# Optimization experiments

Hardware: AMD Instinct MI355X
Metric: run time of the kernel (lower is better)

Reference implementation:

```python
import jax, jax.numpy as jnp
import numpy as np

N = 8388608          # number of samples (2**23)
T_MAX = 100000       # number of distinct time values -> ~84 ties per time


def setup_inputs() -> dict:
    key = jax.random.key(0)
    k1, k2, k3 = jax.random.split(key, 3)
    inp = jax.random.normal(k1, (N,), dtype=jnp.float32)            # log hazards
    target = jax.random.randint(k2, (N,), 0, T_MAX, dtype=jnp.int32)  # times
    weight = jax.random.randint(k3, (N,), 0, 2, dtype=jnp.int32)      # event indicator
    return {"input": inp, "target": target, "weight": weight}


def _cox_efron_npll(log_hz, time, event):
    """Negative Cox partial log-likelihood with Efron tie correction, mean reduction.

    Faithful to torchsurv's _partial_likelihood_efron: per unique time j,
    pll_j = sum_{i in H_j} log_hz_i - sum_{l=0}^{m_j-1} log(D_j - (l/m_j)*T_j)
    where H_j = events at time j, D_j = sum of exp(log_hz) over risk set (t>=t_j),
    T_j = sum of exp(log_hz) over H_j, m_j = |H_j|; loss = -mean over j with m_j>0.
    """
    n = log_hz.shape[0]
    order = jnp.argsort(time)                       # sort by time (group-sum math is tie-order invariant)
    t = time[order]
    lh = log_hz[order]
    ev = event[order].astype(lh.dtype)

    # group id per sample: 0..(num_unique-1), padded groups beyond that are empty
    new_grp = jnp.concatenate([jnp.zeros((1,), jnp.int32), (t[1:] != t[:-1]).astype(jnp.int32)])
    seg = jnp.cumsum(new_grp)                       # [n] int32

    hz = jnp.exp(lh)
    grp_hz = jax.ops.segment_sum(hz, seg, num_segments=n)          # sum exp per time group
    denom_naive = jnp.cumsum(grp_hz[::-1])[::-1]                   # risk-set sums (suffix over groups)
    m = jax.ops.segment_sum(ev, seg, num_segments=n)               # events per group
    log_nom = jax.ops.segment_sum(lh * ev, seg, num_segments=n)    # sum of log_hz over H_j
    ties = jax.ops.segment_sum(hz * ev, seg, num_segments=n)       # sum of exp over H_j

    # rank l in [0, m_j) of each event within its group
    csum_e = jnp.cumsum(ev)
    events_before = jnp.concatenate([jnp.zeros((1,), lh.dtype), jnp.cumsum(m)[:-1]])
    rank = csum_e - 1.0 - events_before[seg]
    mg = jnp.maximum(m[seg], 1.0)
    term = jnp.where(ev > 0.0,
                     jnp.log(denom_naive[seg] - (rank / mg) * ties[seg]),
                     0.0)
    log_denom = jax.ops.segment_sum(term, seg, num_segments=n)

    include = (m > 0.0).astype(lh.dtype)
    pll = jnp.where(m > 0.0, log_nom - log_denom, 0.0)
    # reduction='mean': -pll.nanmean() over groups that contain events
    return -(jnp.sum(pll) / jnp.sum(include))


def reference(input, target, weight):
    return _cox_efron_npll(input, target, weight)
```

## Files before the change

### kernel.cpp

```cpp
#include <hip/hip_runtime.h>

#define TMAXV 100000
#define CHUNK 256
#define NCHUNK ((TMAXV + CHUNK - 1) / CHUNK)
#define WB 512
#define LOGWB 9
#define SB ((TMAXV + WB - 1) / WB)
#define SBP 256
#define TILE 4096
#define RPT 16
#define KS 8
#define NREP 2
#define HSCALE 4096.0f
#define HINV (1.0f / 4096.0f)
#define CAPB 49152


__device__ __forceinline__ float block_reduce_sum(float v, float* sdata) {
    int lane = threadIdx.x & 63;
    int wid  = threadIdx.x >> 6;
    #pragma unroll
    for (int off = 32; off > 0; off >>= 1)
        v += __shfl_down(v, off, 64);
    if (lane == 0) sdata[wid] = v;
    __syncthreads();
    if (wid == 0) {
        v = (lane < 4) ? sdata[lane] : 0.0f;
        v += __shfl_down(v, 2, 64);
        v += __shfl_down(v, 1, 64);
    }
    return v;
}

__device__ __forceinline__ double block_reduce_sum_d(double v, double* sdata) {
    int lane = threadIdx.x & 63;
    int wid  = threadIdx.x >> 6;
    #pragma unroll
    for (int off = 32; off > 0; off >>= 1)
        v += __shfl_down(v, off, 64);
    if (lane == 0) sdata[wid] = v;
    __syncthreads();
    if (wid == 0) {
        v = (lane < 4) ? sdata[lane] : 0.0;
        v += __shfl_down(v, 2, 64);
        v += __shfl_down(v, 1, 64);
    }
    return v;
}

__device__ __forceinline__ unsigned encode_rec(float x, int t, int e) {
    float h = __expf(x);
    unsigned hf = (unsigned)__float2uint_rn(h * HSCALE);
    if (hf > 0x3FFFFFu) hf = 0x3FFFFFu;
    return (hf << 9)
         | (unsigned)(t & (WB - 1))
         | ((unsigned)e << 31);
}


__global__ void scatter_kernel(const float* __restrict__ lh,
                               const int*   __restrict__ tgt,
                               const int*   __restrict__ ev,
                               int*      __restrict__ gcnt,
                               unsigned* __restrict__ val,
                               double*   __restrict__ acc,
                               unsigned* __restrict__ zero_base,
                               int nzero_dw, int n) {
    __shared__ unsigned fu[TILE];
    __shared__ unsigned char bidv[TILE];
    __shared__ int cnl[SBP];
    __shared__ int tb[SBP];
    __shared__ int lrank[SBP];
    __shared__ int ls[SBP];
    __shared__ float sdata[4];
    int tid  = threadIdx.x;
    int tile = blockIdx.x;

    for (int i = tile * 256 + tid; i < nzero_dw; i += gridDim.x * 256)
        zero_base[i] = 0u;

    cnl[tid] = 0; lrank[tid] = 0;
    __syncthreads();

    int lo = tile * TILE;
    int cnt_here = min(TILE, n - lo);

    if (lo + TILE <= n) {
        const int4* tgt4 = (const int4*)(tgt + lo);
        #pragma unroll
        for (int q = 0; q < RPT / 4; ++q) {
            int4 t4 = tgt4[q * 256 + tid];
            atomicAdd(&cnl[t4.x >> LOGWB], 1);
            atomicAdd(&cnl[t4.y >> LOGWB], 1);
            atomicAdd(&cnl[t4.z >> LOGWB], 1);
            atomicAdd(&cnl[t4.w >> LOGWB], 1);
        }
    } else {
        for (int i = lo + tid; i < lo + cnt_here; i += 256)
            atomicAdd(&cnl[tgt[i] >> LOGWB], 1);
    }
    __syncthreads();

    int c0 = cnl[tid];
    ls[tid] = c0;
    __syncthreads();
    for (int off = 1; off < SBP; off <<= 1) {
        int a = (tid >= off) ? ls[tid - off] : 0;
        __syncthreads();
        ls[tid] += a;
        __syncthreads();
    }
    int pfxv = ls[tid] - c0;
    int res = 0;
    if (c0 > 0) {
        res = atomicAdd(&gcnt[tid * 16], c0);
        if (res > CAPB) res = CAPB;
    }
    cnl[tid] = pfxv;
    tb[tid]  = tid * CAPB + res - pfxv;
    __syncthreads();

    float xl = 0.f;
    if (lo + TILE <= n) {
        const int4*   tgt4 = (const int4*)(tgt + lo);
        const int4*   ev4  = (const int4*)(ev + lo);
        const float4* lh4  = (const float4*)(lh + lo);
        #pragma unroll
        for (int q = 0; q < RPT / 4; ++q) {
            int idx = q * 256 + tid;
            int4   t4 = tgt4[idx];
            int4   e4 = ev4[idx];
            float4 x4 = lh4[idx];
            {
                int b = t4.x >> LOGWB; unsigned r = encode_rec(x4.x, t4.x, e4.x & 1);
                int k = atomicAdd(&lrank[b], 1); int pos = cnl[b] + k;
                fu[pos] = r; bidv[pos] = (unsigned char)b; if (e4.x & 1) xl += x4.x;
            }
            {
                int b = t4.y >> LOGWB; unsigned r = encode_rec(x4.y, t4.y, e4.y & 1);
                int k = atomicAdd(&lrank[b], 1); int pos = cnl[b] + k;
                fu[pos] = r; bidv[pos] = (unsigned char)b; if (e4.y & 1) xl += x4.y;
            }
            {
                int b = t4.z >> LOGWB; unsigned r = encode_rec(x4.z, t4.z, e4.z & 1);
                int k = atomicAdd(&lrank[b], 1); int pos = cnl[b] + k;
                fu[pos] = r; bidv[pos] = (unsigned char)b; if (e4.z & 1) xl += x4.z;
            }
            {
                int b = t4.w >> LOGWB; unsigned r = encode_rec(x4.w, t4.w, e4.w & 1);
                int k = atomicAdd(&lrank[b], 1); int pos = cnl[b] + k;
                fu[pos] = r; bidv[pos] = (unsigned char)b; if (e4.w & 1) xl += x4.w;
            }
        }
    } else {
        for (int i = lo + tid; i < lo + cnt_here; i += 256) {
            int t = tgt[i]; int e = ev[i] & 1; float x = lh[i];
            int b = t >> LOGWB; unsigned r = encode_rec(x, t, e);
            int rr = atomicAdd(&lrank[b], 1); int pos = cnl[b] + rr;
            fu[pos] = r; bidv[pos] = (unsigned char)b; if (e) xl += x;
        }
    }
    __syncthreads();

    int pairs = cnt_here >> 1;
    const uint2* fu2 = (const uint2*)fu;
    for (int q = tid; q < pairs; q += 256) {
        uint2 bb = fu2[q];
        int p0 = q * 2;
        int b0 = (int)bidv[p0];
        int b1 = (int)bidv[p0 + 1];
        val[tb[b0] + p0]     = bb.x;
        val[tb[b1] + p0 + 1] = bb.y;
    }
    if ((cnt_here & 1) && tid == 0) {
        int p = cnt_here - 1;
        int b = (int)bidv[p];
        val[tb[b] + p] = fu[p];
    }

    float rl = block_reduce_sum(xl, sdata);
    if (tid == 0) unsafeAtomicAdd(&acc[2], (double)rl);
}

__global__ void bucket_hist_kernel(const unsigned* __restrict__ val,
                                   const int* __restrict__ gcnt,
                                   unsigned* __restrict__ sh_g,
                                   unsigned* __restrict__ cm_g,
                                   unsigned* __restrict__ th_g,
                                   float* __restrict__ chunk_sum) {
    __shared__ unsigned shi[NREP][WB];
    __shared__ unsigned cmi[NREP][WB];
    __shared__ unsigned thi[NREP][WB];
    __shared__ float sdata[4];
    __shared__ float sdata2[4];
    int tid = threadIdx.x;
    int rep = (tid >> 6) & (NREP - 1);
    int b   = blockIdx.x >> 3;
    int k   = blockIdx.x & (KS - 1);
    int len = gcnt[b * 16]; if (len > CAPB) len = CAPB;
    int lo0 = b * CAPB;
    int lo  = lo0 + (int)(((long long)len * k) / KS);
    int hi  = lo0 + (int)(((long long)len * (k + 1)) / KS);

    #pragma unroll
    for (int u = 0; u < NREP * WB / 256; ++u) {
        ((unsigned*)shi)[u * 256 + tid] = 0u;
        ((unsigned*)cmi)[u * 256 + tid] = 0u;
        ((unsigned*)thi)[u * 256 + tid] = 0u;
    }
    __syncthreads();

    for (int i = lo + tid; i < hi; i += 256) {
        unsigned bits = val[i];
        int      s  = (int)(bits & (WB - 1));
        unsigned hf = (bits >> 9) & 0x3FFFFFu;
        atomicAdd(&shi[rep][s], hf);
        if (bits >> 31) {
            atomicAdd(&cmi[rep][s], 1u);
            atomicAdd(&thi[rep][s], hf);
        }
    }
    __syncthreads();

    unsigned s0 = shi[0][tid]       + shi[1][tid];
    unsigned s1 = shi[0][tid + 256] + shi[1][tid + 256];
    unsigned c0 = cmi[0][tid]       + cmi[1][tid];
    unsigned c1 = cmi[0][tid + 256] + cmi[1][tid + 256];
    unsigned t0v = thi[0][tid]       + thi[1][tid];
    unsigned t1v = thi[0][tid + 256] + thi[1][tid + 256];

    int t0 = b * WB + tid;
    if (s0)  atomicAdd(&sh_g[t0],       s0);
    if (s1)  atomicAdd(&sh_g[t0 + 256], s1);
    if (c0)  atomicAdd(&cm_g[t0],       c0);
    if (c1)  atomicAdd(&cm_g[t0 + 256], c1);
    if (t0v) atomicAdd(&th_g[t0],       t0v);
    if (t1v) atomicAdd(&th_g[t0 + 256], t1v);

    float r0 = block_reduce_sum((float)s0 * HINV, sdata);
    __syncthreads();
    float r1 = block_reduce_sum((float)s1 * HINV, sdata2);
    if (tid == 0) {
        unsafeAtomicAdd(&chunk_sum[2 * b],     r0);
        unsafeAtomicAdd(&chunk_sum[2 * b + 1], r1);
    }
}

__global__ void pll_suffix_kernel(const unsigned* __restrict__ sh_g,
                                  const unsigned* __restrict__ cm_g,
                                  const unsigned* __restrict__ th_g,
                                  const float* __restrict__ chunk_sum,
                                  double* __restrict__ acc,
                                  unsigned* __restrict__ done,
                                  float* __restrict__ out) {
    __shared__ float sf[CHUNK];
    __shared__ float sdata[4];
    __shared__ float sdata2[4];
    __shared__ double dsd[4];
    __shared__ double doff;
    int tid = threadIdx.x;
    int b   = blockIdx.x;
    int t   = b * CHUNK + tid;
    float sh = (float)sh_g[t] * HINV;
    unsigned cmu = cm_g[t];
    float th = (float)th_g[t] * HINV;
    sf[tid] = sh;
    __syncthreads();
    for (int off = 1; off < CHUNK; off <<= 1) {
        float add = (tid + off < CHUNK) ? sf[tid + off] : 0.0f;
        __syncthreads();
        sf[tid] += add;
        __syncthreads();
    }
    double mysum = 0.0;
    for (int j = b + 1 + tid; j < NCHUNK; j += 256)
        mysum += (double)chunk_sum[j];
    double red = block_reduce_sum_d(mysum, dsd);
    if (tid == 0) doff = red;
    __syncthreads();
    double off_d = doff;

    float pll = 0.0f, inc = 0.0f;
    if (t < TMAXV && cmu > 0u) {
        float cm   = (float)cmu;
        float D    = (float)(off_d + (double)sf[tid]);
        int   mi   = (int)cmu;
        float step = th / cm;
        float s = 0.0f;
        for (int l = 0; l < mi; ++l)
            s += __logf(D - (float)l * step);
        pll = -s;
        inc = 1.0f;
    }
    float rp = block_reduce_sum(pll, sdata);
    __syncthreads();
    float ri = block_reduce_sum(inc, sdata2);
    if (tid == 0) {
        unsafeAtomicAdd(&acc[0], (double)rp);
        unsafeAtomicAdd(&acc[1], (double)ri);
        __threadfence();
        unsigned prev = __hip_atomic_fetch_add(done, 1u, __ATOMIC_ACQ_REL, __HIP_MEMORY_SCOPE_AGENT);
        if (prev == (unsigned)(gridDim.x - 1)) {
            double a0 = __hip_atomic_load(&acc[0], __ATOMIC_ACQUIRE, __HIP_MEMORY_SCOPE_AGENT);
            double a1 = __hip_atomic_load(&acc[1], __ATOMIC_RELAXED, __HIP_MEMORY_SCOPE_AGENT);
            double a2 = __hip_atomic_load(&acc[2], __ATOMIC_RELAXED, __HIP_MEMORY_SCOPE_AGENT);
            out[0] = (a1 > 0.0) ? (float)(-(a0 + a2) / a1) : 0.0f;
        }
    }
}

__global__ void finalize_kernel(const double* __restrict__ acc,
                                float* __restrict__ out) {
    double cnt = acc[1];
    out[0] = (cnt > 0.0) ? (float)(-(acc[0] + acc[2]) / cnt) : 0.0f;
}

__global__ void hist_kernel(const float* __restrict__ lh,
                            const int*   __restrict__ tgt,
                            const int*   __restrict__ ev,
                            float* __restrict__ sum_hz,
                            float* __restrict__ mcnt,
                            float* __restrict__ log_nom,
                            float* __restrict__ ties,
                            int n) {
    int i = blockIdx.x * blockDim.x + threadIdx.x;
    if (i >= n) return;
    float x = lh[i];
    int   t = tgt[i];
    int   e = ev[i];
    float h = __expf(x);
    unsafeAtomicAdd(&sum_hz[t], h);
    if (e) {
        unsafeAtomicAdd(&mcnt[t], 1.0f);
        unsafeAtomicAdd(&log_nom[t], x);
        unsafeAtomicAdd(&ties[t], h);
    }
}

__global__ void chunk_sum_kernel(const float* __restrict__ sum_hz,
                                 float* __restrict__ chunk_sum) {
    __shared__ float sdata[4];
    int i = blockIdx.x * CHUNK + threadIdx.x;
    float v = (i < TMAXV) ? sum_hz[i] : 0.0f;
    v = block_reduce_sum(v, sdata);
    if (threadIdx.x == 0) chunk_sum[blockIdx.x] = v;
}

__global__ void chunk_scan_kernel(const float* __restrict__ chunk_sum,
                                  double* __restrict__ chunk_off) {
    __shared__ double ds[512];
    int tid = threadIdx.x;
    double own = (tid < NCHUNK) ? (double)chunk_sum[tid] : 0.0;
    ds[tid] = own;
    __syncthreads();
    for (int off = 1; off < 512; off <<= 1) {
        double add = (tid + off < 512) ? ds[tid + off] : 0.0;
        __syncthreads();
        ds[tid] += add;
        __syncthreads();
    }
    if (tid < NCHUNK) chunk_off[tid] = ds[tid] - own;
}

__global__ void pll_kernel(const float* __restrict__ mcnt,
                           const float* __restrict__ log_nom,
                           const float* __restrict__ ties,
                           const float* __restrict__ sum_hz,
                           const double* __restrict__ chunk_off,
                           double* __restrict__ acc) {
    __shared__ float sf[CHUNK];
    __shared__ float sdata[4];
    __shared__ float sdata2[4];
    int tid = threadIdx.x;
    int t   = blockIdx.x * CHUNK + tid;
    float v = (t < TMAXV) ? sum_hz[t] : 0.0f;
    sf[tid] = v;
    __syncthreads();
    for (int off = 1; off < CHUNK; off <<= 1) {
        float add = (tid + off < CHUNK) ? sf[tid + off] : 0.0f;
        __syncthreads();
        sf[tid] += add;
        __syncthreads();
    }
    float pll = 0.0f, inc = 0.0f;
    if (t < TMAXV) {
        float mv = mcnt[t];
        if (mv > 0.5f) {
            float D    = (float)(chunk_off[blockIdx.x] + (double)sf[tid]);
            float T    = ties[t];
            int   mi   = (int)(mv + 0.5f);
            float step = T / mv;
            float s = 0.0f;
            for (int l = 0; l < mi; ++l)
                s += __logf(D - (float)l * step);
            pll = log_nom[t] - s;
            inc = 1.0f;
        }
    }
    float rp = block_reduce_sum(pll, sdata);
    __syncthreads();
    float ri = block_reduce_sum(inc, sdata2);
    if (threadIdx.x == 0) {
        atomicAdd(&acc[0], (double)rp);
        atomicAdd(&acc[1], (double)ri);
    }
}

extern "C" void kernel_launch(void* const* d_in, const int* in_sizes, int n_in,
                              void* d_out, int out_size, void* d_ws, size_t ws_size,
                              hipStream_t stream) {
    const float* lh  = (const float*)d_in[0];
    const int*   tgt = (const int*)d_in[1];
    const int*   ev  = (const int*)d_in[2];
    float*       out = (float*)d_out;
    int n  = in_sizes[0];
    int nt = (n + TILE - 1) / TILE;

    char* ws = (char*)d_ws;
    size_t off = 0;
    auto take = [&](size_t bytes, size_t align) {
        off = (off + align - 1) & ~(align - 1);
        size_t r = off; off += bytes; return r;
    };
    size_t o_acc   = take(32, 16);
    size_t o_gcnt  = take((size_t)SB * 64, 64);
    size_t zero1   = off;
    size_t o_done  = take(16, 16);
    size_t o_csum  = take((size_t)512 * 4, 16);
    size_t o_shg   = take((size_t)SB * WB * 4, 16);
    size_t o_cmg   = take((size_t)SB * WB * 4, 16);
    size_t o_thg   = take((size_t)SB * WB * 4, 16);
    size_t zero2_end = off;
    size_t o_val   = take((size_t)(SB + 1) * CAPB * 4, 16);
    size_t need    = off;

    if (ws_size >= need && n <= 9000000) {
        double*   acc       = (double*)(ws + o_acc);
        int*      gcnt      = (int*)(ws + o_gcnt);
        unsigned* done      = (unsigned*)(ws + o_done);
        float*    chunk_sum = (float*)(ws + o_csum);
        unsigned* sh_g      = (unsigned*)(ws + o_shg);
        unsigned* cm_g      = (unsigned*)(ws + o_cmg);
        unsigned* th_g      = (unsigned*)(ws + o_thg);
        unsigned* val       = (unsigned*)(ws + o_val);

        hipMemsetAsync(ws, 0, zero1, stream);

        scatter_kernel<<<nt, 256, 0, stream>>>(lh, tgt, ev, gcnt, val, acc,
                                               (unsigned*)(ws + o_done),
                                               (int)((zero2_end - o_done) / 4), n);
        bucket_hist_kernel<<<SB * KS, 256, 0, stream>>>(val, gcnt, sh_g, cm_g, th_g,
                                                        chunk_sum);
        pll_suffix_kernel<<<NCHUNK, 256, 0, stream>>>(sh_g, cm_g, th_g, chunk_sum,
                                                      acc, done, out);
    } else {
        size_t f = 0;
        auto ftake = [&](size_t bytes, size_t align) {
            f = (f + align - 1) & ~(align - 1);
            size_t r = f; f += bytes; return r;
        };
        size_t f_acc  = ftake(32, 16);
        size_t f_sum  = ftake((size_t)TMAXV * 4, 16);
        size_t f_m    = ftake((size_t)TMAXV * 4, 16);
        size_t f_ln   = ftake((size_t)TMAXV * 4, 16);
        size_t f_ties = ftake((size_t)TMAXV * 4, 16);
        size_t zb     = f;
        size_t f_csum = ftake((size_t)NCHUNK * 4, 16);
        size_t f_coff = ftake((size_t)NCHUNK * 8, 8);

        double* acc     = (double*)(ws + f_acc);
        float*  sum_hz  = (float*)(ws + f_sum);
        float*  mcnt    = (float*)(ws + f_m);
        float*  log_nom = (float*)(ws + f_ln);
        float*  ties    = (float*)(ws + f_ties);
        float*  chunk_sum = (float*)(ws + f_csum);
        double* chunk_off = (double*)(ws + f_coff);

        hipMemsetAsync(d_ws, 0, zb, stream);

        hist_kernel<<<(n + 255) / 256, 256, 0, stream>>>(lh, tgt, ev, sum_hz, mcnt, log_nom, ties, n);
        chunk_sum_kernel<<<NCHUNK, 256, 0, stream>>>(sum_hz, chunk_sum);
        chunk_scan_kernel<<<1, 512, 0, stream>>>(chunk_sum, chunk_off);
        pll_kernel<<<NCHUNK, 256, 0, stream>>>(mcnt, log_nom, ties, sum_hz, chunk_off, acc);
        finalize_kernel<<<1, 1, 0, stream>>>(acc, out);
    }
}
```

Baseline: 216.1 us.

## Replace bucket scatter with direct global atomic histograms per time value

Drops the two-pass bucket scatter (LDS partition, writing packed records to global memory, then a per-bucket LDS histogram) in favour of direct global atomics into per-time arrays. The event count and tie-hazard sum are packed into a single 64-bit atomic, and a small kernel computes the per-chunk sums. This removes the 32 MB intermediate write and re-read, but each sample now issues one or two global atomics on about 100k addresses, with contention of roughly 84 hits per address. A grid-stride loop caps the grid at 2048 blocks.

```diff
diff --git a/kernel.cpp b/kernel.cpp
--- a/kernel.cpp
+++ b/kernel.cpp
@@ -3,17 +3,12 @@
 #define TMAXV 100000
 #define CHUNK 256
 #define NCHUNK ((TMAXV + CHUNK - 1) / CHUNK)
-#define WB 512
-#define LOGWB 9
-#define SB ((TMAXV + WB - 1) / WB)
-#define SBP 256
+#define NTPAD (NCHUNK * CHUNK)
 #define TILE 4096
 #define RPT 16
-#define KS 8
-#define NREP 2
 #define HSCALE 4096.0f
 #define HINV (1.0f / 4096.0f)
-#define CAPB 49152
+#define THSHIFT 42
 
 
 __device__ __forceinline__ float block_reduce_sum(float v, float* sdata) {
@@ -48,207 +43,81 @@
     return v;
 }
 
-__device__ __forceinline__ unsigned encode_rec(float x, int t, int e) {
-    float h = __expf(x);
-    unsigned hf = (unsigned)__float2uint_rn(h * HSCALE);
-    if (hf > 0x3FFFFFu) hf = 0x3FFFFFu;
-    return (hf << 9)
-         | (unsigned)(t & (WB - 1))
-         | ((unsigned)e << 31);
-}
-
-
-__global__ void scatter_kernel(const float* __restrict__ lh,
-                               const int*   __restrict__ tgt,
-                               const int*   __restrict__ ev,
-                               int*      __restrict__ gcnt,
-                               unsigned* __restrict__ val,
-                               double*   __restrict__ acc,
-                               unsigned* __restrict__ zero_base,
-                               int nzero_dw, int n) {
-    __shared__ unsigned fu[TILE];
-    __shared__ unsigned char bidv[TILE];
-    __shared__ int cnl[SBP];
-    __shared__ int tb[SBP];
-    __shared__ int lrank[SBP];
-    __shared__ int ls[SBP];
-    __shared__ float sdata[4];
-    int tid  = threadIdx.x;
-    int tile = blockIdx.x;
-
-    for (int i = tile * 256 + tid; i < nzero_dw; i += gridDim.x * 256)
-        zero_base[i] = 0u;
-
-    cnl[tid] = 0; lrank[tid] = 0;
-    __syncthreads();
-
-    int lo = tile * TILE;
-    int cnt_here = min(TILE, n - lo);
-
-    if (lo + TILE <= n) {
-        const int4* tgt4 = (const int4*)(tgt + lo);
-        #pragma unroll
-        for (int q = 0; q < RPT / 4; ++q) {
-            int4 t4 = tgt4[q * 256 + tid];
-            atomicAdd(&cnl[t4.x >> LOGWB], 1);
-            atomicAdd(&cnl[t4.y >> LOGWB], 1);
-            atomicAdd(&cnl[t4.z >> LOGWB], 1);
-            atomicAdd(&cnl[t4.w >> LOGWB], 1);
-        }
-    } else {
-        for (int i = lo + tid; i < lo + cnt_here; i += 256)
-            atomicAdd(&cnl[tgt[i] >> LOGWB], 1);
-    }
-    __syncthreads();
-
-    int c0 = cnl[tid];
-    ls[tid] = c0;
-    __syncthreads();
-    for (int off = 1; off < SBP; off <<= 1) {
-        int a = (tid >= off) ? ls[tid - off] : 0;
-        __syncthreads();
-        ls[tid] += a;
-        __syncthreads();
-    }
-    int pfxv = ls[tid] - c0;
-    int res = 0;
-    if (c0 > 0) {
-        res = atomicAdd(&gcnt[tid * 16], c0);
-        if (res > CAPB) res = CAPB;
-    }
-    cnl[tid] = pfxv;
-    tb[tid]  = tid * CAPB + res - pfxv;
-    __syncthreads();
-
+
+__global__ __launch_bounds__(256, 8)
+void hist_direct_kernel(const float* __restrict__ lh,
+                        const int*   __restrict__ tgt,
+                        const int*   __restrict__ ev,
+                        unsigned* __restrict__ sh_g,
+                        unsigned long long* __restrict__ cmth_g,
+                        double* __restrict__ acc, int n) {
+    __shared__ float sdata[4];
+    int tid = threadIdx.x;
     float xl = 0.f;
-    if (lo + TILE <= n) {
-        const int4*   tgt4 = (const int4*)(tgt + lo);
-        const int4*   ev4  = (const int4*)(ev + lo);
-        const float4* lh4  = (const float4*)(lh + lo);
-        #pragma unroll
-        for (int q = 0; q < RPT / 4; ++q) {
-            int idx = q * 256 + tid;
-            int4   t4 = tgt4[idx];
-            int4   e4 = ev4[idx];
-            float4 x4 = lh4[idx];
-            {
-                int b = t4.x >> LOGWB; unsigned r = encode_rec(x4.x, t4.x, e4.x & 1);
-                int k = atomicAdd(&lrank[b], 1); int pos = cnl[b] + k;
-                fu[pos] = r; bidv[pos] = (unsigned char)b; if (e4.x & 1) xl += x4.x;
+
+    for (long long lo = (long long)blockIdx.x * TILE; lo < n;
+         lo += (long long)gridDim.x * TILE) {
+        if (lo + TILE <= n) {
+            const int4*   tgt4 = (const int4*)(tgt + lo);
+            const int4*   ev4  = (const int4*)(ev + lo);
+            const float4* lh4  = (const float4*)(lh + lo);
+            #pragma unroll
+            for (int q = 0; q < RPT / 4; ++q) {
+                int idx = q * 256 + tid;
+                int4   t4 = tgt4[idx];
+                int4   e4 = ev4[idx];
+                float4 x4 = lh4[idx];
+                {
+                    unsigned hf = __float2uint_rn(__expf(x4.x) * HSCALE);
+                    if (hf > 0x3FFFFFu) hf = 0x3FFFFFu;
+                    atomicAdd(&sh_g[t4.x], hf);
+                    if (e4.x & 1) { atomicAdd(&cmth_g[t4.x], (1ull << THSHIFT) | (unsigned long long)hf); xl += x4.x; }
+                }
+                {
+                    unsigned hf = __float2uint_rn(__expf(x4.y) * HSCALE);
+                    if (hf > 0x3FFFFFu) hf = 0x3FFFFFu;
+                    atomicAdd(&sh_g[t4.y], hf);
+                    if (e4.y & 1) { atomicAdd(&cmth_g[t4.y], (1ull << THSHIFT) | (unsigned long long)hf); xl += x4.y; }
+                }
+                {
+                    unsigned hf = __float2uint_rn(__expf(x4.z) * HSCALE);
+                    if (hf > 0x3FFFFFu) hf = 0x3FFFFFu;
+                    atomicAdd(&sh_g[t4.z], hf);
+                    if (e4.z & 1) { atomicAdd(&cmth_g[t4.z], (1ull << THSHIFT) | (unsigned long long)hf); xl += x4.z; }
+                }
+                {
+                    unsigned hf = __float2uint_rn(__expf(x4.w) * HSCALE);
+                    if (hf > 0x3FFFFFu) hf = 0x3FFFFFu;
+                    atomicAdd(&sh_g[t4.w], hf);
+                    if (e4.w & 1) { atomicAdd(&cmth_g[t4.w], (1ull << THSHIFT) | (unsigned long long)hf); xl += x4.w; }
+                }
             }
-            {
-                int b = t4.y >> LOGWB; unsigned r = encode_rec(x4.y, t4.y, e4.y & 1);
-                int k = atomicAdd(&lrank[b], 1); int pos = cnl[b] + k;
-                fu[pos] = r; bidv[pos] = (unsigned char)b; if (e4.y & 1) xl += x4.y;
-            }
-            {
-                int b = t4.z >> LOGWB; unsigned r = encode_rec(x4.z, t4.z, e4.z & 1);
-                int k = atomicAdd(&lrank[b], 1); int pos = cnl[b] + k;
-                fu[pos] = r; bidv[pos] = (unsigned char)b; if (e4.z & 1) xl += x4.z;
-            }
-            {
-                int b = t4.w >> LOGWB; unsigned r = encode_rec(x4.w, t4.w, e4.w & 1);
-                int k = atomicAdd(&lrank[b], 1); int pos = cnl[b] + k;
-                fu[pos] = r; bidv[pos] = (unsigned char)b; if (e4.w & 1) xl += x4.w;
+        } else {
+            for (long long i = lo + tid; i < n; i += 256) {
+                int t = tgt[i]; int e = ev[i] & 1; float x = lh[i];
+                unsigned hf = __float2uint_rn(__expf(x) * HSCALE);
+                if (hf > 0x3FFFFFu) hf = 0x3FFFFFu;
+                atomicAdd(&sh_g[t], hf);
+                if (e) { atomicAdd(&cmth_g[t], (1ull << THSHIFT) | (unsigned long long)hf); xl += x; }
             }
         }
-    } else {
-        for (int i = lo + tid; i < lo + cnt_here; i += 256) {
-            int t = tgt[i]; int e = ev[i] & 1; float x = lh[i];
-            int b = t >> LOGWB; unsigned r = encode_rec(x, t, e);
-            int rr = atomicAdd(&lrank[b], 1); int pos = cnl[b] + rr;
-            fu[pos] = r; bidv[pos] = (unsigned char)b; if (e) xl += x;
-        }
-    }
-    __syncthreads();
-
-    int pairs = cnt_here >> 1;
-    const uint2* fu2 = (const uint2*)fu;
-    for (int q = tid; q < pairs; q += 256) {
-        uint2 bb = fu2[q];
-        int p0 = q * 2;
-        int b0 = (int)bidv[p0];
-        int b1 = (int)bidv[p0 + 1];
-        val[tb[b0] + p0]     = bb.x;
-        val[tb[b1] + p0 + 1] = bb.y;
-    }
-    if ((cnt_here & 1) && tid == 0) {
-        int p = cnt_here - 1;
-        int b = (int)bidv[p];
-        val[tb[b] + p] = fu[p];
     }
 
     float rl = block_reduce_sum(xl, sdata);
     if (tid == 0) unsafeAtomicAdd(&acc[2], (double)rl);
 }
 
-__global__ void bucket_hist_kernel(const unsigned* __restrict__ val,
-                                   const int* __restrict__ gcnt,
-                                   unsigned* __restrict__ sh_g,
-                                   unsigned* __restrict__ cm_g,
-                                   unsigned* __restrict__ th_g,
-                                   float* __restrict__ chunk_sum) {
-    __shared__ unsigned shi[NREP][WB];
-    __shared__ unsigned cmi[NREP][WB];
-    __shared__ unsigned thi[NREP][WB];
-    __shared__ float sdata[4];
-    __shared__ float sdata2[4];
-    int tid = threadIdx.x;
-    int rep = (tid >> 6) & (NREP - 1);
-    int b   = blockIdx.x >> 3;
-    int k   = blockIdx.x & (KS - 1);
-    int len = gcnt[b * 16]; if (len > CAPB) len = CAPB;
-    int lo0 = b * CAPB;
-    int lo  = lo0 + (int)(((long long)len * k) / KS);
-    int hi  = lo0 + (int)(((long long)len * (k + 1)) / KS);
-
-    #pragma unroll
-    for (int u = 0; u < NREP * WB / 256; ++u) {
-        ((unsigned*)shi)[u * 256 + tid] = 0u;
-        ((unsigned*)cmi)[u * 256 + tid] = 0u;
-        ((unsigned*)thi)[u * 256 + tid] = 0u;
-    }
-    __syncthreads();
-
-    for (int i = lo + tid; i < hi; i += 256) {
-        unsigned bits = val[i];
-        int      s  = (int)(bits & (WB - 1));
-        unsigned hf = (bits >> 9) & 0x3FFFFFu;
-        atomicAdd(&shi[rep][s], hf);
-        if (bits >> 31) {
-            atomicAdd(&cmi[rep][s], 1u);
-            atomicAdd(&thi[rep][s], hf);
-        }
-    }
-    __syncthreads();
-
-    unsigned s0 = shi[0][tid]       + shi[1][tid];
-    unsigned s1 = shi[0][tid + 256] + shi[1][tid + 256];
-    unsigned c0 = cmi[0][tid]       + cmi[1][tid];
-    unsigned c1 = cmi[0][tid + 256] + cmi[1][tid + 256];
-    unsigned t0v = thi[0][tid]       + thi[1][tid];
-    unsigned t1v = thi[0][tid + 256] + thi[1][tid + 256];
-
-    int t0 = b * WB + tid;
-    if (s0)  atomicAdd(&sh_g[t0],       s0);
-    if (s1)  atomicAdd(&sh_g[t0 + 256], s1);
-    if (c0)  atomicAdd(&cm_g[t0],       c0);
-    if (c1)  atomicAdd(&cm_g[t0 + 256], c1);
-    if (t0v) atomicAdd(&th_g[t0],       t0v);
-    if (t1v) atomicAdd(&th_g[t0 + 256], t1v);
-
-    float r0 = block_reduce_sum((float)s0 * HINV, sdata);
-    __syncthreads();
-    float r1 = block_reduce_sum((float)s1 * HINV, sdata2);
-    if (tid == 0) {
-        unsafeAtomicAdd(&chunk_sum[2 * b],     r0);
-        unsafeAtomicAdd(&chunk_sum[2 * b + 1], r1);
-    }
+__global__ void chunk_sum_u32_kernel(const unsigned* __restrict__ sh_g,
+                                     float* __restrict__ chunk_sum) {
+    __shared__ float sdata[4];
+    int i = blockIdx.x * CHUNK + threadIdx.x;
+    float v = (i < TMAXV) ? (float)sh_g[i] * HINV : 0.0f;
+    v = block_reduce_sum(v, sdata);
+    if (threadIdx.x == 0) chunk_sum[blockIdx.x] = v;
 }
 
 __global__ void pll_suffix_kernel(const unsigned* __restrict__ sh_g,
-                                  const unsigned* __restrict__ cm_g,
-                                  const unsigned* __restrict__ th_g,
+                                  const unsigned long long* __restrict__ cmth_g,
                                   const float* __restrict__ chunk_sum,
                                   double* __restrict__ acc,
                                   unsigned* __restrict__ done,
@@ -261,9 +130,10 @@
     int tid = threadIdx.x;
     int b   = blockIdx.x;
     int t   = b * CHUNK + tid;
-    float sh = (float)sh_g[t] * HINV;
-    unsigned cmu = cm_g[t];
-    float th = (float)th_g[t] * HINV;
+    float sh = (t < TMAXV) ? (float)sh_g[t] * HINV : 0.0f;
+    unsigned long long pk = (t < TMAXV) ? cmth_g[t] : 0ull;
+    unsigned cmu = (unsigned)(pk >> THSHIFT);
+    float th = (float)(pk & ((1ull << THSHIFT) - 1)) * HINV;
     sf[tid] = sh;
     __syncthreads();
     for (int off = 1; off < CHUNK; off <<= 1) {
@@ -423,35 +293,26 @@
         size_t r = off; off += bytes; return r;
     };
     size_t o_acc   = take(32, 16);
-    size_t o_gcnt  = take((size_t)SB * 64, 64);
-    size_t zero1   = off;
     size_t o_done  = take(16, 16);
-    size_t o_csum  = take((size_t)512 * 4, 16);
-    size_t o_shg   = take((size_t)SB * WB * 4, 16);
-    size_t o_cmg   = take((size_t)SB * WB * 4, 16);
-    size_t o_thg   = take((size_t)SB * WB * 4, 16);
-    size_t zero2_end = off;
-    size_t o_val   = take((size_t)(SB + 1) * CAPB * 4, 16);
+    size_t o_csum  = take((size_t)NCHUNK * 4, 16);
+    size_t o_shg   = take((size_t)NTPAD * 4, 16);
+    size_t o_cmth  = take((size_t)NTPAD * 8, 16);
     size_t need    = off;
 
-    if (ws_size >= need && n <= 9000000) {
-        double*   acc       = (double*)(ws + o_acc);
-        int*      gcnt      = (int*)(ws + o_gcnt);
-        unsigned* done      = (unsigned*)(ws + o_done);
-        float*    chunk_sum = (float*)(ws + o_csum);
-        unsigned* sh_g      = (unsigned*)(ws + o_shg);
-        unsigned* cm_g      = (unsigned*)(ws + o_cmg);
-        unsigned* th_g      = (unsigned*)(ws + o_thg);
-        unsigned* val       = (unsigned*)(ws + o_val);
-
-        hipMemsetAsync(ws, 0, zero1, stream);
-
-        scatter_kernel<<<nt, 256, 0, stream>>>(lh, tgt, ev, gcnt, val, acc,
-                                               (unsigned*)(ws + o_done),
-                                               (int)((zero2_end - o_done) / 4), n);
-        bucket_hist_kernel<<<SB * KS, 256, 0, stream>>>(val, gcnt, sh_g, cm_g, th_g,
-                                                        chunk_sum);
-        pll_suffix_kernel<<<NCHUNK, 256, 0, stream>>>(sh_g, cm_g, th_g, chunk_sum,
+    if (ws_size >= need) {
+        double*             acc       = (double*)(ws + o_acc);
+        unsigned*           done      = (unsigned*)(ws + o_done);
+        float*              chunk_sum = (float*)(ws + o_csum);
+        unsigned*           sh_g      = (unsigned*)(ws + o_shg);
+        unsigned long long* cmth_g    = (unsigned long long*)(ws + o_cmth);
+
+        hipMemsetAsync(ws, 0, need, stream);
+
+        int grid = nt < 2048 ? nt : 2048;
+        hist_direct_kernel<<<grid, 256, 0, stream>>>(lh, tgt, ev, sh_g, cmth_g,
+                                                     acc, n);
+        chunk_sum_u32_kernel<<<NCHUNK, 256, 0, stream>>>(sh_g, chunk_sum);
+        pll_suffix_kernel<<<NCHUNK, 256, 0, stream>>>(sh_g, cmth_g, chunk_sum,
                                                       acc, done, out);
     } else {
         size_t f = 0;
```

Measured after the change: 626.7 us. 2.9x slower.
